# Performance work log

Measured on AMD Instinct MI355X. Metric: run time of the kernel, lower is better.

## Reference

```python
import jax, jax.numpy as jnp
import numpy as np

D_MODEL = 1024
N_HEADS = 16
D_KEY = D_MODEL // N_HEADS
NEG = -1e9


def setup_inputs() -> dict:
    key = jax.random.key(0)
    ks = jax.random.split(key, 10)
    B, S = 4, 2048
    s = 0.02
    query = jax.random.normal(ks[0], (B, S, D_MODEL), dtype=jnp.float32)
    # causal mask: 1 where attend allowed, 0 where masked (masked_fill(mask==0, -1e9))
    mask = jnp.tril(jnp.ones((S, S), dtype=jnp.int32))[None, None]
    Wq = jax.random.normal(ks[1], (D_MODEL, D_MODEL), dtype=jnp.float32) * s
    bq = jax.random.normal(ks[2], (D_MODEL,), dtype=jnp.float32) * s
    Wk = jax.random.normal(ks[3], (D_MODEL, D_MODEL), dtype=jnp.float32) * s
    bk = jax.random.normal(ks[4], (D_MODEL,), dtype=jnp.float32) * s
    Wv = jax.random.normal(ks[5], (D_MODEL, D_MODEL), dtype=jnp.float32) * s
    bv = jax.random.normal(ks[6], (D_MODEL,), dtype=jnp.float32) * s
    Wo = jax.random.normal(ks[7], (D_MODEL, D_MODEL), dtype=jnp.float32) * s
    bo = jax.random.normal(ks[8], (D_MODEL,), dtype=jnp.float32) * s
    return {"query": query, "mask": mask, "Wq": Wq, "bq": bq, "Wk": Wk,
            "bk": bk, "Wv": Wv, "bv": bv, "Wo": Wo, "bo": bo}


def _split_heads(x):
    B, S, _ = x.shape
    return x.reshape(B, S, N_HEADS, D_KEY).transpose(0, 2, 1, 3)  # [B,H,S,Dk]


def reference(query, mask, Wq, bq, Wk, bk, Wv, bv, Wo, bo):
    B, S, _ = query.shape
    # torch Linear: x @ W^T + b
    q = _split_heads(query @ Wq.T + bq)
    k = _split_heads(query @ Wk.T + bk)  # self-attention: key_value is None
    v = _split_heads(query @ Wv.T + bv)
    scores = jnp.einsum('bhqd,bhkd->bhqk', q, k) / jnp.sqrt(jnp.float32(D_KEY))
    scores = jnp.where(mask == 0, jnp.float32(NEG), scores)
    weights = jax.nn.softmax(scores, axis=-1)  # dropout=0 (eval)
    attn = jnp.einsum('bhqk,bhkd->bhqd', weights, v)
    merged = attn.transpose(0, 2, 1, 3).reshape(B, S, D_MODEL)
    return merged @ Wo.T + bo
```

## Files before the change

### kernel.cpp

```cpp
#include <hip/hip_runtime.h>
#include <hip/hip_bf16.h>

typedef __attribute__((ext_vector_type(8))) short bf16x8;
typedef __attribute__((ext_vector_type(4))) float f32x4;
typedef __attribute__((ext_vector_type(16))) float f32x16;
typedef __attribute__((ext_vector_type(2))) unsigned int u32x2;

__device__ __forceinline__ float fexp2(float x) { return __builtin_amdgcn_exp2f(x); }

__device__ __forceinline__ ushort f2bf(float x) {
    union { float f; unsigned u; } c; c.f = x;
    unsigned r = c.u + 0x7fff + ((c.u >> 16) & 1);
    return (ushort)(r >> 16);
}

__device__ __forceinline__ unsigned cvtpk(float lo, float hi) {
    unsigned r;
    asm("v_cvt_pk_bf16_f32 %0, %1, %2" : "=v"(r) : "v"(lo), "v"(hi));
    return r;
}

__device__ __forceinline__ void gload16(const void* g, void* l) {
    __builtin_amdgcn_global_load_lds((const __attribute__((address_space(1))) void*)g,
                                     (__attribute__((address_space(3))) void*)l, 16, 0, 0);
}

__device__ __forceinline__ void blockbar() {
    asm volatile("" ::: "memory");
    __builtin_amdgcn_s_barrier();
    asm volatile("" ::: "memory");
}

template<int N> __device__ __forceinline__ void vmwait() {
    if constexpr (N == 9)      asm volatile("s_waitcnt vmcnt(9)" ::: "memory");
    else if constexpr (N == 6) asm volatile("s_waitcnt vmcnt(6)" ::: "memory");
    else if constexpr (N == 3) asm volatile("s_waitcnt vmcnt(3)" ::: "memory");
    else                       asm volatile("s_waitcnt vmcnt(0)" ::: "memory");
}

__global__ void cvt_f32_bf16(const float* __restrict__ in, ushort* __restrict__ out, int n4) {
    int i = blockIdx.x * blockDim.x + threadIdx.x;
    int stride = gridDim.x * blockDim.x;
    for (; i < n4; i += stride) {
        float4 v = ((const float4*)in)[i];
        ushort4 o;
        o.x = f2bf(v.x); o.y = f2bf(v.y); o.z = f2bf(v.z); o.w = f2bf(v.w);
        ((ushort4*)out)[i] = o;
    }
}

__global__ void cvt_w4(const float* __restrict__ a, const float* __restrict__ b,
                       const float* __restrict__ c, const float* __restrict__ d,
                       ushort* __restrict__ oq, ushort* __restrict__ ow) {
    const int N4 = 262144;
    int i = blockIdx.x * blockDim.x + threadIdx.x;
    int stride = gridDim.x * blockDim.x;
    for (; i < 4 * N4; i += stride) {
        int sel = i >> 18, local = i & (N4 - 1);
        const float* src = (sel == 0) ? a : (sel == 1) ? b : (sel == 2) ? c : d;
        float4 v = ((const float4*)src)[local];
        ushort4 o;
        o.x = f2bf(v.x); o.y = f2bf(v.y); o.z = f2bf(v.z); o.w = f2bf(v.w);
        if (sel < 3) ((ushort4*)oq)[sel * N4 + local] = o;
        else         ((ushort4*)ow)[local] = o;
    }
}

template<int MODE>
__global__ __launch_bounds__(512, 2)
void gemm_8p(const ushort* __restrict__ A, const ushort* __restrict__ Bt,
             const float* __restrict__ bias0, const float* __restrict__ bias1,
             const float* __restrict__ bias2,
             ushort* __restrict__ outb, float* __restrict__ outf,
             int M, int N, int K) {
    __shared__ ushort lds[49152];
    const int t = threadIdx.x, lane = t & 63, w = t >> 6;
    const int wm = w >> 1, wn = w & 1;
    const int l15 = lane & 15, lg = lane >> 4;
    const int asw = (l15 >> 1) & 3;

    const int nbx = N >> 7;
    const int nwg = nbx * (M >> 8);
    const int bid = blockIdx.y * nbx + blockIdx.x;
    const int swz = (bid & 7) * (nwg >> 3) + (bid >> 3);
    const int m0 = (swz / nbx) * 256, n0 = (swz % nbx) * 128;

    const int srow = lane >> 2;
    const int sblk = (lane & 3) ^ ((lane >> 3) & 3);
    const ushort* Asrc0 = A + (size_t)(m0 + 16 * w + srow) * K + sblk * 8;
    const ushort* Asrc1 = A + (size_t)(m0 + 128 + 16 * w + srow) * K + sblk * 8;
    const ushort* Bsrc  = Bt + (size_t)(n0 + 16 * w + srow) * K + sblk * 8;
    ushort* ldsA0 = &lds[w * 512];
    ushort* ldsA1 = &lds[(8 + w) * 512];
    ushort* ldsB  = &lds[8192 + w * 512];

#define STAGE(ST, KT) { \
    gload16(Asrc0 + (KT) * 32, ldsA0 + (ST) * 12288); \
    gload16(Asrc1 + (KT) * 32, ldsA1 + (ST) * 12288); \
    gload16(Bsrc  + (KT) * 32, ldsB  + (ST) * 12288); }

    const int abase = (wm * 64 + l15) * 32 + ((lg ^ asw) << 3);
    const int bbase = 8192 + (wn * 64 + l15) * 32 + ((lg ^ asw) << 3);

    f32x4 acc[4][4] = {};
    const int NT = K >> 5;

    STAGE(0, 0); STAGE(1, 1); STAGE(2, 2);

    for (int kt = 0; kt < NT; ++kt) {
        if (kt + 3 < NT) STAGE((kt + 3) & 3, kt + 3);
        const int ahead = NT - 1 - kt;
        if (ahead >= 3) vmwait<9>();
        else if (ahead == 2) vmwait<6>();
        else if (ahead == 1) vmwait<3>();
        else vmwait<0>();
        blockbar();

        const ushort* sa = lds + (kt & 3) * 12288 + abase;
        const ushort* sb = lds + (kt & 3) * 12288 + bbase;
        bf16x8 af[4], bfr[4];
#pragma unroll
        for (int mi = 0; mi < 4; mi++) af[mi] = *(const bf16x8*)(sa + mi * 512);
#pragma unroll
        for (int ni = 0; ni < 4; ni++) bfr[ni] = *(const bf16x8*)(sb + ni * 512);

        __builtin_amdgcn_s_setprio(1);
#pragma unroll
        for (int mi = 0; mi < 4; mi++)
#pragma unroll
            for (int ni = 0; ni < 4; ni++)
                acc[mi][ni] = __builtin_amdgcn_mfma_f32_16x16x32_bf16(af[mi], bfr[ni], acc[mi][ni], 0, 0, 0);
        __builtin_amdgcn_s_setprio(0);
        blockbar();
    }
#undef STAGE

#pragma unroll
    for (int mi = 0; mi < 4; mi++)
#pragma unroll
        for (int ni = 0; ni < 4; ni++)
#pragma unroll
            for (int r = 0; r < 4; r++) {
                int gm = m0 + wm * 64 + mi * 16 + lg * 4 + r;
                int gn = n0 + wn * 64 + ni * 16 + l15;
                if (MODE == 0) {
                    const float* bp = (gn < 1024) ? bias0 : ((gn < 2048) ? bias1 : bias2);
                    float v = acc[mi][ni][r] + bp[gn & 1023];
                    if (gn < 1024) v *= 0.18033688011f;
                    int proj = gn >> 10, nn = gn & 1023;
                    int h = nn >> 6, d = nn & 63;
                    int b = gm >> 11, s = gm & 2047;
                    outb[(size_t)proj * 8388608 + ((((size_t)b << 4) + h) * 2048 + s) * 64 + d] = f2bf(v);
                } else {
                    outf[(size_t)gm * N + gn] = acc[mi][ni][r] + bias0[gn];
                }
            }
}

__global__ __launch_bounds__(256, 3)
void attn_fwd(const ushort* __restrict__ Qb, const ushort* __restrict__ Kb,
              const ushort* __restrict__ Vb, ushort* __restrict__ Ab) {
    constexpr int S = 2048;
    __shared__ ushort lds[16384];

    const int bid = blockIdx.x;
    const int qt = 15 - (bid >> 6);
    const int bh = bid & 63;
    const int b = bh >> 4, h = bh & 15;
    const ushort* Qp = Qb + (size_t)bh * S * 64;
    const ushort* Kp = Kb + (size_t)bh * S * 64;
    const ushort* Vp = Vb + (size_t)bh * S * 64;

    const int t = threadIdx.x, lane = t & 63, w = t >> 6;
    const int l15 = lane & 15, l31 = lane & 31, hi = lane >> 5, g = lane >> 4;

    int koff[2], voff[2];
#pragma unroll
    for (int i = 0; i < 2; i++) {
        int row = (w * 2 + i) * 8 + (lane >> 3);
        int gg = (lane & 7) ^ ((row ^ (row >> 3)) & 7);
        koff[i] = row * 64 + gg * 8;
    }
#pragma unroll
    for (int it = 0; it < 2; it++) {
        int T = (it * 4 + w) * 64 + lane;
        int kvb = T >> 5, db = (T >> 3) & 3, kvr = (T >> 1) & 3, dh = T & 1;
        voff[it] = (kvb * 4 + kvr) * 64 + db * 16 + dh * 8;
    }
    const unsigned vtbase = (unsigned)(uintptr_t)&lds[8192]
                          + (hi << 10) + ((g & 1) << 7) + (l15 << 3);

    auto stage = [&](int phase, int k0) {
#pragma unroll
        for (int i = 0; i < 2; i++)
            gload16(Kp + (size_t)k0 * 64 + koff[i], &lds[(phase << 12) + ((w * 2 + i) << 9)]);
#pragma unroll
        for (int it = 0; it < 2; it++)
            gload16(Vp + (size_t)k0 * 64 + voff[it], &lds[8192 + (phase << 12) + (((it << 2) + w) << 9)]);
    };

    const int fb = qt * 128 + w * 32;
    const int nt = 2 * qt + 2;

    bf16x8 qf[4];
#pragma unroll
    for (int kc = 0; kc < 4; kc++)
        qf[kc] = *(const bf16x8*)&Qp[(size_t)(fb + l31) * 64 + kc * 16 + hi * 8];

    float m = -3e38f, ls = 0.f;
    f32x16 O0 = {}, O1 = {};

    stage(0, 0);

    for (int tile = 0; tile < nt; tile++) {
        const int phase = tile & 1;
        const int k0 = tile * 64;
        if (tile + 1 < nt) {
            stage(phase ^ 1, (tile + 1) * 64);
            asm volatile("s_waitcnt vmcnt(4)" ::: "memory");
        } else {
            asm volatile("s_waitcnt vmcnt(0)" ::: "memory");
        }
        blockbar();

        if (k0 <= fb + 31) {
            const ushort* Kc = &lds[phase << 12];
            f32x16 s0 = {}, s1 = {};
            {
                bf16x8 kf[4];
#pragma unroll
                for (int kc = 0; kc < 4; kc++) {
                    int row = l31;
                    int sw = (row ^ (row >> 3)) & 7;
                    kf[kc] = *(const bf16x8*)&Kc[row * 64 + (((kc * 2 + hi) ^ sw) << 3)];
                }
                __builtin_amdgcn_s_setprio(1);
#pragma unroll
                for (int kc = 0; kc < 4; kc++)
                    s0 = __builtin_amdgcn_mfma_f32_32x32x16_bf16(kf[kc], qf[kc], s0, 0, 0, 0);
                __builtin_amdgcn_s_setprio(0);
            }
            {
                bf16x8 kf[4];
#pragma unroll
                for (int kc = 0; kc < 4; kc++) {
                    int row = 32 + l31;
                    int sw = (row ^ (row >> 3)) & 7;
                    kf[kc] = *(const bf16x8*)&Kc[row * 64 + (((kc * 2 + hi) ^ sw) << 3)];
                }
                __builtin_amdgcn_s_setprio(1);
#pragma unroll
                for (int kc = 0; kc < 4; kc++)
                    s1 = __builtin_amdgcn_mfma_f32_32x32x16_bf16(kf[kc], qf[kc], s1, 0, 0, 0);
                __builtin_amdgcn_s_setprio(0);
            }

            float pv[32];
            const bool diag = (k0 + 63 > fb);
            const int rel = fb + l31 - k0 - 4 * hi;
#pragma unroll
            for (int r = 0; r < 16; r++) {
                float v0 = s0[r], v1 = s1[r];
                if (diag) {
                    int kvc = (r & 3) + 8 * (r >> 2);
                    if (kvc > rel)      v0 = -1e30f;
                    if (kvc + 32 > rel) v1 = -1e30f;
                }
                pv[r] = v0; pv[16 + r] = v1;
            }
            float mx[16];
#pragma unroll
            for (int i = 0; i < 16; i++) mx[i] = fmaxf(pv[i], pv[i + 16]);
#pragma unroll
            for (int sgap = 8; sgap >= 1; sgap >>= 1)
#pragma unroll
                for (int i = 0; i < sgap; i++) mx[i] = fmaxf(mx[i], mx[i + sgap]);
            float pmax = fmaxf(mx[0], __shfl_xor(mx[0], 32));

            if (!__all(pmax <= m + 8.f)) {
                float mnew = fmaxf(m, pmax);
                float a = fexp2(m - mnew);
                ls *= a;
                float ar[16];
#pragma unroll
                for (int r = 0; r < 16; r++)
                    ar[r] = __shfl(a, (r & 3) + 8 * (r >> 2) + 4 * hi, 32);
#pragma unroll
                for (int r = 0; r < 16; r++) { O0[r] *= ar[r]; O1[r] *= ar[r]; }
                m = mnew;
            }
#pragma unroll
            for (int i = 0; i < 32; i++) pv[i] = fexp2(pv[i] - m);
            float sm[16];
#pragma unroll
            for (int i = 0; i < 16; i++) sm[i] = pv[i] + pv[i + 16];
#pragma unroll
            for (int sgap = 8; sgap >= 1; sgap >>= 1)
#pragma unroll
                for (int i = 0; i < sgap; i++) sm[i] += sm[i + sgap];
            ls += sm[0] + __shfl_xor(sm[0], 32);

            union PAu { bf16x8 v; unsigned wd[4]; } PA[4];
#pragma unroll
            for (int ks = 0; ks < 4; ks++)
#pragma unroll
                for (int i = 0; i < 2; i++) {
                    unsigned xw = cvtpk(pv[8 * ks + 2 * i], pv[8 * ks + 2 * i + 1]);
                    unsigned yw = cvtpk(pv[8 * ks + 2 * i + 4], pv[8 * ks + 2 * i + 5]);
                    asm("v_permlane32_swap_b32 %0, %1" : "+v"(xw), "+v"(yw));
                    PA[ks].wd[i] = xw; PA[ks].wd[2 + i] = yw;
                }

            const unsigned vtb = vtbase + (phase << 13);
            u32x2 vb[16];
#define TRR(idx, OFFSTR) asm volatile("ds_read_b64_tr_b16 %0, %1 offset:" OFFSTR : "=v"(vb[idx]) : "v"(vtb))
            TRR(0, "0");    TRR(1, "512");  TRR(2, "2048"); TRR(3, "2560");
            TRR(4, "4096"); TRR(5, "4608"); TRR(6, "6144"); TRR(7, "6656");
            TRR(8, "256");  TRR(9, "768");  TRR(10, "2304"); TRR(11, "2816");
            TRR(12, "4352"); TRR(13, "4864"); TRR(14, "6400"); TRR(15, "6912");
#undef TRR
            union FragU { bf16x8 v; u32x2 hh[2]; };
            asm volatile("s_waitcnt lgkmcnt(8)" ::: "memory");
            __builtin_amdgcn_sched_barrier(0);
            __builtin_amdgcn_s_setprio(1);
#pragma unroll
            for (int ks = 0; ks < 4; ks++) {
                FragU f; f.hh[0] = vb[ks * 2]; f.hh[1] = vb[ks * 2 + 1];
                O0 = __builtin_amdgcn_mfma_f32_32x32x16_bf16(PA[ks].v, f.v, O0, 0, 0, 0);
            }
            __builtin_amdgcn_s_setprio(0);
            asm volatile("s_waitcnt lgkmcnt(0)" ::: "memory");
            __builtin_amdgcn_sched_barrier(0);
            __builtin_amdgcn_s_setprio(1);
#pragma unroll
            for (int ks = 0; ks < 4; ks++) {
                FragU f; f.hh[0] = vb[8 + ks * 2]; f.hh[1] = vb[8 + ks * 2 + 1];
                O1 = __builtin_amdgcn_mfma_f32_32x32x16_bf16(PA[ks].v, f.v, O1, 0, 0, 0);
            }
            __builtin_amdgcn_s_setprio(0);
        }
        blockbar();
    }

    float inv[16];
#pragma unroll
    for (int r = 0; r < 16; r++)
        inv[r] = __builtin_amdgcn_rcpf(__shfl(ls, (r & 3) + 8 * (r >> 2) + 4 * hi, 32));
#pragma unroll
    for (int r = 0; r < 16; r++) {
        int q = fb + (r & 3) + 8 * (r >> 2) + 4 * hi;
        size_t base = ((size_t)b * 2048 + q) * 1024 + h * 64;
        Ab[base + l31]      = f2bf(O0[r] * inv[r]);
        Ab[base + 32 + l31] = f2bf(O1[r] * inv[r]);
    }
}

extern "C" void kernel_launch(void* const* d_in, const int* in_sizes, int n_in,
                              void* d_out, int out_size, void* d_ws, size_t ws_size,
                              hipStream_t stream) {
    const float* query = (const float*)d_in[0];
    const float* Wq = (const float*)d_in[2];
    const float* bq = (const float*)d_in[3];
    const float* Wk = (const float*)d_in[4];
    const float* bk = (const float*)d_in[5];
    const float* Wv = (const float*)d_in[6];
    const float* bv = (const float*)d_in[7];
    const float* Wo = (const float*)d_in[8];
    const float* bo = (const float*)d_in[9];
    float* out = (float*)d_out;

    char* ws = (char*)d_ws;
    const size_t SZ_X = 8192ull * 1024 * 2;
    const size_t SZ_W = 1024ull * 1024 * 2;
    ushort* Xb   = (ushort*)(ws);
    ushort* Wcat = (ushort*)(ws + SZ_X);
    ushort* Wob  = (ushort*)(ws + SZ_X + 3 * SZ_W);
    ushort* QKVb = (ushort*)(ws + SZ_X + 4 * SZ_W);
    ushort* Ab   = (ushort*)(ws + 4 * SZ_X + 4 * SZ_W);

    cvt_f32_bf16<<<1024, 256, 0, stream>>>(query, Xb, 8192 * 1024 / 4);
    cvt_w4<<<1024, 256, 0, stream>>>(Wq, Wk, Wv, Wo, Wcat, Wob);

    gemm_8p<0><<<dim3(3072 / 128, 8192 / 256), 512, 0, stream>>>(
        Xb, Wcat, bq, bk, bv, QKVb, nullptr, 8192, 3072, 1024);

    attn_fwd<<<1024, 256, 0, stream>>>(QKVb, QKVb + 8388608, QKVb + 2 * 8388608, Ab);

    gemm_8p<1><<<dim3(1024 / 128, 8192 / 256), 512, 0, stream>>>(
        Ab, Wob, bo, nullptr, nullptr, nullptr, out, 8192, 1024, 1024);
}
```

Before: 174.6 us.

## Restructure GEMM to double-buffered BK=64 stages with mid-tile prefetch

Changes the GEMM mainloop from a 4-stage BK=32 LDS ring to a 2-stage BK=64 ring. The next tile load is issued after the first half of the MFMAs, once both fragment halves are in registers. LDS rows widen to 64 elements with an 8-way XOR swizzle, and each wave issues six 16-byte global-to-LDS loads per stage. The aim is to halve barriers and loop overhead per K element. The cost is shallower prefetch depth and more fragment registers.

```diff
diff --git a/kernel.cpp b/kernel.cpp
--- a/kernel.cpp
+++ b/kernel.cpp
@@ -29,13 +29,6 @@
     asm volatile("" ::: "memory");
     __builtin_amdgcn_s_barrier();
     asm volatile("" ::: "memory");
-}
-
-template<int N> __device__ __forceinline__ void vmwait() {
-    if constexpr (N == 9)      asm volatile("s_waitcnt vmcnt(9)" ::: "memory");
-    else if constexpr (N == 6) asm volatile("s_waitcnt vmcnt(6)" ::: "memory");
-    else if constexpr (N == 3) asm volatile("s_waitcnt vmcnt(3)" ::: "memory");
-    else                       asm volatile("s_waitcnt vmcnt(0)" ::: "memory");
 }
 
 __global__ void cvt_f32_bf16(const float* __restrict__ in, ushort* __restrict__ out, int n4) {
@@ -68,7 +61,7 @@
 
 template<int MODE>
 __global__ __launch_bounds__(512, 2)
-void gemm_8p(const ushort* __restrict__ A, const ushort* __restrict__ Bt,
+void gemm_p2(const ushort* __restrict__ A, const ushort* __restrict__ Bt,
              const float* __restrict__ bias0, const float* __restrict__ bias1,
              const float* __restrict__ bias2,
              ushort* __restrict__ outb, float* __restrict__ outf,
@@ -77,7 +70,7 @@
     const int t = threadIdx.x, lane = t & 63, w = t >> 6;
     const int wm = w >> 1, wn = w & 1;
     const int l15 = lane & 15, lg = lane >> 4;
-    const int asw = (l15 >> 1) & 3;
+    const int sw7 = l15 & 7;
 
     const int nbx = N >> 7;
     const int nwg = nbx * (M >> 8);
@@ -85,53 +78,69 @@
     const int swz = (bid & 7) * (nwg >> 3) + (bid >> 3);
     const int m0 = (swz / nbx) * 256, n0 = (swz % nbx) * 128;
 
-    const int srow = lane >> 2;
-    const int sblk = (lane & 3) ^ ((lane >> 3) & 3);
-    const ushort* Asrc0 = A + (size_t)(m0 + 16 * w + srow) * K + sblk * 8;
-    const ushort* Asrc1 = A + (size_t)(m0 + 128 + 16 * w + srow) * K + sblk * 8;
-    const ushort* Bsrc  = Bt + (size_t)(n0 + 16 * w + srow) * K + sblk * 8;
-    ushort* ldsA0 = &lds[w * 512];
-    ushort* ldsA1 = &lds[(8 + w) * 512];
-    ushort* ldsB  = &lds[8192 + w * 512];
+    const int srow = lane >> 3;
+    const int gcb = (lane & 7) ^ srow;
+    const ushort* gsrc[6];
+#pragma unroll
+    for (int s = 0; s < 4; s++)
+        gsrc[s] = A + (size_t)(m0 + s * 64 + w * 8 + srow) * K + gcb * 8;
+#pragma unroll
+    for (int s = 0; s < 2; s++)
+        gsrc[4 + s] = Bt + (size_t)(n0 + s * 64 + w * 8 + srow) * K + gcb * 8;
 
 #define STAGE(ST, KT) { \
-    gload16(Asrc0 + (KT) * 32, ldsA0 + (ST) * 12288); \
-    gload16(Asrc1 + (KT) * 32, ldsA1 + (ST) * 12288); \
-    gload16(Bsrc  + (KT) * 32, ldsB  + (ST) * 12288); }
-
-    const int abase = (wm * 64 + l15) * 32 + ((lg ^ asw) << 3);
-    const int bbase = 8192 + (wn * 64 + l15) * 32 + ((lg ^ asw) << 3);
+    ushort* dst = &lds[(ST) * 24576 + w * 512]; \
+    gload16(gsrc[0] + (KT) * 64, dst); \
+    gload16(gsrc[1] + (KT) * 64, dst + 4096); \
+    gload16(gsrc[2] + (KT) * 64, dst + 8192); \
+    gload16(gsrc[3] + (KT) * 64, dst + 12288); \
+    gload16(gsrc[4] + (KT) * 64, dst + 16384); \
+    gload16(gsrc[5] + (KT) * 64, dst + 20480); }
 
     f32x4 acc[4][4] = {};
-    const int NT = K >> 5;
-
-    STAGE(0, 0); STAGE(1, 1); STAGE(2, 2);
+    const int NT = K >> 6;
+
+    STAGE(0, 0); STAGE(1, 1);
 
     for (int kt = 0; kt < NT; ++kt) {
-        if (kt + 3 < NT) STAGE((kt + 3) & 3, kt + 3);
-        const int ahead = NT - 1 - kt;
-        if (ahead >= 3) vmwait<9>();
-        else if (ahead == 2) vmwait<6>();
-        else if (ahead == 1) vmwait<3>();
-        else vmwait<0>();
+        if (kt < NT - 1) asm volatile("s_waitcnt vmcnt(6)" ::: "memory");
+        else             asm volatile("s_waitcnt vmcnt(0)" ::: "memory");
         blockbar();
 
-        const ushort* sa = lds + (kt & 3) * 12288 + abase;
-        const ushort* sb = lds + (kt & 3) * 12288 + bbase;
-        bf16x8 af[4], bfr[4];
-#pragma unroll
-        for (int mi = 0; mi < 4; mi++) af[mi] = *(const bf16x8*)(sa + mi * 512);
-#pragma unroll
-        for (int ni = 0; ni < 4; ni++) bfr[ni] = *(const bf16x8*)(sb + ni * 512);
+        const ushort* stg = &lds[(kt & 1) * 24576];
+        bf16x8 a0[4], b0[4], a1[4], b1[4];
+#pragma unroll
+        for (int mi = 0; mi < 4; mi++) {
+            int row = wm * 64 + mi * 16 + l15;
+            a0[mi] = *(const bf16x8*)&stg[row * 64 + ((lg ^ sw7) << 3)];
+            a1[mi] = *(const bf16x8*)&stg[row * 64 + (((4 + lg) ^ sw7) << 3)];
+        }
+#pragma unroll
+        for (int ni = 0; ni < 4; ni++) {
+            int row = wn * 64 + ni * 16 + l15;
+            b0[ni] = *(const bf16x8*)&stg[16384 + row * 64 + ((lg ^ sw7) << 3)];
+            b1[ni] = *(const bf16x8*)&stg[16384 + row * 64 + (((4 + lg) ^ sw7) << 3)];
+        }
 
         __builtin_amdgcn_s_setprio(1);
 #pragma unroll
         for (int mi = 0; mi < 4; mi++)
 #pragma unroll
             for (int ni = 0; ni < 4; ni++)
-                acc[mi][ni] = __builtin_amdgcn_mfma_f32_16x16x32_bf16(af[mi], bfr[ni], acc[mi][ni], 0, 0, 0);
+                acc[mi][ni] = __builtin_amdgcn_mfma_f32_16x16x32_bf16(a0[mi], b0[ni], acc[mi][ni], 0, 0, 0);
         __builtin_amdgcn_s_setprio(0);
+
+        asm volatile("s_waitcnt lgkmcnt(0)" ::: "memory");
         blockbar();
+        if (kt + 2 < NT) STAGE((kt & 1), kt + 2);
+
+        __builtin_amdgcn_s_setprio(1);
+#pragma unroll
+        for (int mi = 0; mi < 4; mi++)
+#pragma unroll
+            for (int ni = 0; ni < 4; ni++)
+                acc[mi][ni] = __builtin_amdgcn_mfma_f32_16x16x32_bf16(a1[mi], b1[ni], acc[mi][ni], 0, 0, 0);
+        __builtin_amdgcn_s_setprio(0);
     }
 #undef STAGE
 
@@ -381,11 +390,11 @@
     cvt_f32_bf16<<<1024, 256, 0, stream>>>(query, Xb, 8192 * 1024 / 4);
     cvt_w4<<<1024, 256, 0, stream>>>(Wq, Wk, Wv, Wo, Wcat, Wob);
 
-    gemm_8p<0><<<dim3(3072 / 128, 8192 / 256), 512, 0, stream>>>(
+    gemm_p2<0><<<dim3(3072 / 128, 8192 / 256), 512, 0, stream>>>(
         Xb, Wcat, bq, bk, bv, QKVb, nullptr, 8192, 3072, 1024);
 
     attn_fwd<<<1024, 256, 0, stream>>>(QKVb, QKVb + 8388608, QKVb + 2 * 8388608, Ab);
 
-    gemm_8p<1><<<dim3(1024 / 128, 8192 / 256), 512, 0, stream>>>(
+    gemm_p2<1><<<dim3(1024 / 128, 8192 / 256), 512, 0, stream>>>(
         Ab, Wob, bo, nullptr, nullptr, nullptr, out, 8192, 1024, 1024);
 }
```

Result: faster. 164.8 us (-5.6%).
